# Optimization experiments

Measured on AMD Instinct MI355X. Metric: run time of the kernel, lower is better.

## Reference

```python
import jax, jax.numpy as jnp
import numpy as np

B, H, W, C = 4, 64, 64, 256
CK = C // 8          # 32, f/g projection dim
COUT = 256           # channels_out


def setup_inputs() -> dict:
    key = jax.random.key(0)
    ks = jax.random.split(key, 6)
    s = lambda fan_in: 1.0 / np.sqrt(fan_in)
    return {
        "x": jax.random.normal(ks[0], (B, H, W, C), dtype=jnp.float32),
        "Wf": jax.random.normal(ks[1], (C, CK), dtype=jnp.float32) * s(C),
        "bf": jnp.zeros((CK,), dtype=jnp.float32),
        "Wg": jax.random.normal(ks[2], (C, CK), dtype=jnp.float32) * s(C),
        "bg": jnp.zeros((CK,), dtype=jnp.float32),
        "Wh": jax.random.normal(ks[3], (C, COUT), dtype=jnp.float32) * s(C),
        "bh": jnp.zeros((COUT,), dtype=jnp.float32),
        "Wo": jax.random.normal(ks[4], (COUT, COUT), dtype=jnp.float32) * s(COUT),
        "bo": jnp.zeros((COUT,), dtype=jnp.float32),
        "gamma": jnp.zeros((1,), dtype=jnp.float32),
    }


def reference(x, Wf, bf, Wg, bg, Wh, bh, Wo, bo, gamma):
    b, h, w, c = x.shape
    n = h * w
    xf = x.reshape(b, n, c)                       # [B, N, C]
    # 1x1 convs == per-location dense projections
    f = xf @ Wf + bf                              # [B, N, CK]
    g = xf @ Wg + bg                              # [B, N, CK]
    hh = xf @ Wh + bh                             # [B, N, COUT]
    scores = jnp.einsum("bqk,bnk->bqn", f, g)    # [B, N, N]
    probs = jax.nn.softmax(scores, axis=-1)
    attn = jnp.einsum("bqn,bnd->bqd", probs, hh)  # [B, N, COUT]
    o = attn @ Wo + bo                            # [B, N, COUT]
    y = gamma * o.reshape(b, h, w, -1) + x
    return y
```

## Files before the change

kernel.cpp:

```cpp
#include <hip/hip_runtime.h>
#include <stdint.h>

typedef __attribute__((ext_vector_type(4))) float f32x4;
typedef __attribute__((ext_vector_type(2))) float f32x2;
typedef __attribute__((ext_vector_type(8))) short bf16x8;
typedef __attribute__((ext_vector_type(4))) unsigned short u16x4;

#define NB 4
#define NN 4096
#define CC 256

__device__ __forceinline__ unsigned short f2bf(float f) {
  union { float f; unsigned int u; } v; v.f = f;
  unsigned int u = v.u;
  return (unsigned short)((u + 0x7FFFu + ((u >> 16) & 1u)) >> 16);
}
__device__ __forceinline__ float bf2f(unsigned short h) {
  union { unsigned int u; float f; } v; v.u = ((unsigned int)h) << 16;
  return v.f;
}

typedef __attribute__((address_space(1))) void as1_void;
typedef __attribute__((address_space(3))) void as3_void;
__device__ __forceinline__ void gload_lds16(const unsigned short* g, unsigned short* l) {
  __builtin_amdgcn_global_load_lds((as1_void*)(void*)g, (as3_void*)(void*)l, 16, 0, 0);
}

__global__ __launch_bounds__(64) void k_wprep(
    const float* __restrict__ Wf, const float* __restrict__ Wg,
    const float* __restrict__ Wh, const float* __restrict__ Wo,
    unsigned short* __restrict__ wT, unsigned short* __restrict__ woT)
{
  const int n = blockIdx.x;
  const int l = threadIdx.x;
  const float* src; int nout, col; unsigned short* dst; int drow;
  if (n < 32)       { src = Wf; nout = 32;  col = n;       dst = wT;  drow = n; }
  else if (n < 64)  { src = Wg; nout = 32;  col = n - 32;  dst = wT;  drow = n; }
  else if (n < 320) { src = Wh; nout = 256; col = n - 64;  dst = wT;  drow = n; }
  else              { src = Wo; nout = 256; col = n - 320; dst = woT; drow = n - 320; }
  u16x4 v;
  #pragma unroll
  for (int j = 0; j < 4; ++j)
    v[j] = f2bf(src[(size_t)(4 * l + j) * nout + col]);
  *(u16x4*)&dst[(size_t)drow * 256 + 4 * l] = v;
}

__global__ __launch_bounds__(256) void k_proj(
    const float* __restrict__ x, const unsigned short* __restrict__ wT,
    const float* __restrict__ bf_, const float* __restrict__ bg_,
    const float* __restrict__ bh_,
    unsigned short* __restrict__ fo, unsigned short* __restrict__ go,
    unsigned short* __restrict__ vT)
{
  __shared__ __align__(16) unsigned short xs[32][264];

  const int t = threadIdx.x, w = t >> 6, l = t & 63;
  const int h = l >> 4, q = l & 15;
  const int bid = blockIdx.x;
  const int rt = (bid & 7) * 64 + (bid >> 3);
  const int r0 = rt * 32;

  #pragma unroll
  for (int p = 0; p < 8; ++p) {
    int idx = t + (p << 8);
    int rr = idx >> 6, c4 = (idx & 63) << 2;
    f32x4 v = *(const f32x4*)&x[(size_t)(r0 + rr) * 256 + c4];
    u16x4 o;
    #pragma unroll
    for (int j = 0; j < 4; ++j) o[j] = f2bf(v[j]);
    *(u16x4*)&xs[rr][c4] = o;
  }
  __syncthreads();

  const f32x4 zero = {0.f, 0.f, 0.f, 0.f};
  f32x4 acc[2][5];
  #pragma unroll
  for (int mf = 0; mf < 2; ++mf)
    #pragma unroll
    for (int nf = 0; nf < 5; ++nf) acc[mf][nf] = zero;

  #pragma unroll
  for (int ks = 0; ks < 8; ++ks) {
    bf16x8 a0 = *(const bf16x8*)&xs[q][ks * 32 + 8 * h];
    bf16x8 a1 = *(const bf16x8*)&xs[16 + q][ks * 32 + 8 * h];
    #pragma unroll
    for (int nf = 0; nf < 5; ++nf) {
      bf16x8 b = *(const bf16x8*)&wT[(size_t)(80 * w + 16 * nf + q) * 256 + ks * 32 + 8 * h];
      acc[0][nf] = __builtin_amdgcn_mfma_f32_16x16x32_bf16(a0, b, acc[0][nf], 0, 0, 0);
      acc[1][nf] = __builtin_amdgcn_mfma_f32_16x16x32_bf16(a1, b, acc[1][nf], 0, 0, 0);
    }
  }

  __syncthreads();

  #pragma unroll
  for (int nf = 0; nf < 5; ++nf) {
    const int colb = 80 * w + 16 * nf;
    const int colq = colb + q;
    #pragma unroll
    for (int mf = 0; mf < 2; ++mf) {
      #pragma unroll
      for (int i = 0; i < 4; ++i) {
        int lr = 16 * mf + 4 * h + i;
        float val = acc[mf][nf][i];
        if (colb < 32) {
          fo[(size_t)(r0 + lr) * 32 + colq] =
              f2bf((val + bf_[colq]) * 1.44269504088896f);
        } else if (colb < 64) {
          go[(size_t)(r0 + lr) * 32 + (colq - 32)] = f2bf(val + bg_[colq - 32]);
        } else {
          xs[lr][colq - 64] = f2bf(val + bh_[colq - 64]);
        }
      }
    }
  }
  __syncthreads();

  const int tile = rt >> 1, sfix = rt & 1;
  unsigned short* dst = vT + (size_t)tile * 16384;
  #pragma unroll
  for (int p = 0; p < 4; ++p) {
    int ci = t + (p << 8);
    int dt = ci >> 6, ll = ci & 63;
    int h2 = (ci >> 4) & 3, q2 = ci & 15;
    bf16x8 v;
    #pragma unroll
    for (int i = 0; i < 8; ++i)
      v[i] = (short)xs[8 * h2 + i][dt * 16 + q2];
    *(bf16x8*)&dst[(size_t)(dt * 128 + sfix * 64 + ll) * 8] = v;
  }
}

#define SM_FIXED_MAX 72.0f

__global__ __launch_bounds__(256, 2) void k_attn(
    const unsigned short* __restrict__ fq,
    const unsigned short* __restrict__ gk,
    const unsigned short* __restrict__ vT,
    float* __restrict__ attn)
{
  __shared__ __align__(16) unsigned short vbuf[2][16384];
  __shared__ __align__(16) unsigned short pbuf[2][2048];
  __shared__ float lred[4][2][16];

  const int bid = blockIdx.x;
  const int b  = (bid & 7) >> 1;
  const int qt = (bid >> 3) + ((bid & 1) << 6);
  const int t = threadIdx.x, w = t >> 6, l = t & 63;
  const int h = l >> 4, q = l & 15;
  const int qrow = qt * 32;

  bf16x8 afrag[2];
  #pragma unroll
  for (int u = 0; u < 2; ++u)
    afrag[u] = *(const bf16x8*)&fq[((size_t)b * NN + qrow + u * 16 + q) * 32 + 8 * h];

  const f32x4 zero = {0.f, 0.f, 0.f, 0.f};
  f32x4 acc[2][4];
  #pragma unroll
  for (int u = 0; u < 2; ++u)
    #pragma unroll
    for (int dl = 0; dl < 4; ++dl) acc[u][dl] = zero;
  float lrow[2][4];
  #pragma unroll
  for (int u = 0; u < 2; ++u)
    #pragma unroll
    for (int i = 0; i < 4; ++i) lrow[u][i] = 0.f;

  const unsigned short* gbase = gk + (size_t)b * NN * 32;
  const unsigned short* vbase = vT + (size_t)b * 64 * 16384;

  const int kcol = w * 16 + q;
  const int ps = kcol >> 5, ph2 = (kcol & 31) >> 3, pi2 = kcol & 7;

  {
    const unsigned short* src = vbase + (size_t)w * 4096 + l * 8;
    unsigned short* dst = &vbuf[0][w * 4096];
    #pragma unroll
    for (int i2 = 0; i2 < 8; ++i2)
      gload_lds16(src + i2 * 512, dst + i2 * 512);
  }
  bf16x8 bfj = *(const bf16x8*)&gbase[(size_t)(w * 16 + q) * 32 + 8 * h];
  __syncthreads();

  #pragma unroll 1
  for (int kt = 0; kt < 64; ++kt) {
    const int cur = kt & 1;

    f32x4 s0 = __builtin_amdgcn_mfma_f32_16x16x32_bf16(afrag[0], bfj, zero, 0, 0, 0);
    f32x4 s1 = __builtin_amdgcn_mfma_f32_16x16x32_bf16(afrag[1], bfj, zero, 0, 0, 0);

    bf16x8 bfn = bfj;
    if (kt < 63)
      bfn = *(const bf16x8*)&gbase[(size_t)((kt + 1) * 64 + w * 16 + q) * 32 + 8 * h];

    #pragma unroll
    for (int i = 0; i < 4; ++i) {
      float p0 = exp2f(s0[i] - SM_FIXED_MAX);
      float p1 = exp2f(s1[i] - SM_FIXED_MAX);
      lrow[0][i] += p0;
      lrow[1][i] += p1;
      int slot = (ph2 * 16 + 4 * h + i) * 8 + pi2;
      pbuf[cur][(0 + ps) * 512 + slot] = (unsigned short)(__float_as_uint(p0) >> 16);
      pbuf[cur][(2 + ps) * 512 + slot] = (unsigned short)(__float_as_uint(p1) >> 16);
    }

    __syncthreads();

    if (kt < 63) {
      const unsigned short* src = vbase + (size_t)(kt + 1) * 16384 + w * 4096 + l * 8;
      unsigned short* dst = &vbuf[cur ^ 1][w * 4096];
      #pragma unroll
      for (int i2 = 0; i2 < 8; ++i2)
        gload_lds16(src + i2 * 512, dst + i2 * 512);
    }

    bf16x8 pa[2][2];
    #pragma unroll
    for (int u = 0; u < 2; ++u)
      #pragma unroll
      for (int s2 = 0; s2 < 2; ++s2)
        pa[u][s2] = *(const bf16x8*)&pbuf[cur][(u * 2 + s2) * 512 + l * 8];

    __builtin_amdgcn_s_setprio(1);
    #pragma unroll
    for (int dl = 0; dl < 4; ++dl) {
      const int dt = 4 * w + dl;
      bf16x8 v0 = *(const bf16x8*)&vbuf[cur][dt * 1024 + l * 8];
      bf16x8 v1 = *(const bf16x8*)&vbuf[cur][dt * 1024 + 512 + l * 8];
      acc[0][dl] = __builtin_amdgcn_mfma_f32_16x16x32_bf16(pa[0][0], v0, acc[0][dl], 0, 0, 0);
      acc[1][dl] = __builtin_amdgcn_mfma_f32_16x16x32_bf16(pa[1][0], v0, acc[1][dl], 0, 0, 0);
      acc[0][dl] = __builtin_amdgcn_mfma_f32_16x16x32_bf16(pa[0][1], v1, acc[0][dl], 0, 0, 0);
      acc[1][dl] = __builtin_amdgcn_mfma_f32_16x16x32_bf16(pa[1][1], v1, acc[1][dl], 0, 0, 0);
    }
    __builtin_amdgcn_s_setprio(0);

    bfj = bfn;
  }

  #pragma unroll
  for (int u = 0; u < 2; ++u)
    #pragma unroll
    for (int i = 0; i < 4; ++i)
      #pragma unroll
      for (int d = 1; d < 16; d <<= 1)
        lrow[u][i] += __shfl_xor(lrow[u][i], d);

  if (q == 0) {
    #pragma unroll
    for (int u = 0; u < 2; ++u)
      #pragma unroll
      for (int i = 0; i < 4; ++i)
        lred[w][u][4 * h + i] = lrow[u][i];
  }
  __syncthreads();

  float rl[2][4];
  #pragma unroll
  for (int u = 0; u < 2; ++u)
    #pragma unroll
    for (int i = 0; i < 4; ++i) {
      int row = 4 * h + i;
      rl[u][i] = 1.0f / (lred[0][u][row] + lred[1][u][row] +
                         lred[2][u][row] + lred[3][u][row]);
    }

  #pragma unroll
  for (int u = 0; u < 2; ++u)
    #pragma unroll
    for (int dl = 0; dl < 4; ++dl) {
      int dt = 4 * w + dl;
      #pragma unroll
      for (int i = 0; i < 4; ++i)
        attn[((size_t)b * NN + qrow + u * 16 + 4 * h + i) * 256 + dt * 16 + q] =
            acc[u][dl][i] * rl[u][i];
    }
}

__global__ __launch_bounds__(256) void k_out(
    const unsigned short* __restrict__ woT, const float* __restrict__ bo,
    const float* __restrict__ gamma, const float* __restrict__ x,
    float* __restrict__ y)
{
  __shared__ __align__(16) unsigned short as_[32][264];

  const int t = threadIdx.x, w = t >> 6, l = t & 63;
  const int h = l >> 4, q = l & 15;
  const int bid = blockIdx.x;
  const int rt = (bid & 7) * 64 + (bid >> 3);
  const int r0 = rt * 32;

  #pragma unroll
  for (int p = 0; p < 8; ++p) {
    int idx = t + (p << 8);
    int rr = idx >> 6, c4 = (idx & 63) << 2;
    f32x4 v = *(const f32x4*)&y[(size_t)(r0 + rr) * 256 + c4];
    u16x4 o;
    #pragma unroll
    for (int j = 0; j < 4; ++j) o[j] = f2bf(v[j]);
    *(u16x4*)&as_[rr][c4] = o;
  }
  __syncthreads();

  const f32x4 zero = {0.f, 0.f, 0.f, 0.f};
  f32x4 acc[2][4];
  #pragma unroll
  for (int mf = 0; mf < 2; ++mf)
    #pragma unroll
    for (int nf = 0; nf < 4; ++nf) acc[mf][nf] = zero;

  #pragma unroll
  for (int ks = 0; ks < 8; ++ks) {
    bf16x8 a0 = *(const bf16x8*)&as_[q][ks * 32 + 8 * h];
    bf16x8 a1 = *(const bf16x8*)&as_[16 + q][ks * 32 + 8 * h];
    #pragma unroll
    for (int nf = 0; nf < 4; ++nf) {
      bf16x8 b = *(const bf16x8*)&woT[(size_t)(64 * w + 16 * nf + q) * 256 + ks * 32 + 8 * h];
      acc[0][nf] = __builtin_amdgcn_mfma_f32_16x16x32_bf16(a0, b, acc[0][nf], 0, 0, 0);
      acc[1][nf] = __builtin_amdgcn_mfma_f32_16x16x32_bf16(a1, b, acc[1][nf], 0, 0, 0);
    }
  }

  const float gm = gamma[0];
  #pragma unroll
  for (int mf = 0; mf < 2; ++mf)
    #pragma unroll
    for (int nf = 0; nf < 4; ++nf) {
      int col = 64 * w + 16 * nf + q;
      #pragma unroll
      for (int i = 0; i < 4; ++i) {
        size_t off = (size_t)(r0 + 16 * mf + 4 * h + i) * 256 + col;
        y[off] = gm * (acc[mf][nf][i] + bo[col]) + x[off];
      }
    }
}

extern "C" void kernel_launch(void* const* d_in, const int* in_sizes, int n_in,
                              void* d_out, int out_size, void* d_ws, size_t ws_size,
                              hipStream_t stream) {
  const float* x     = (const float*)d_in[0];
  const float* Wf    = (const float*)d_in[1];
  const float* bf_   = (const float*)d_in[2];
  const float* Wg    = (const float*)d_in[3];
  const float* bg_   = (const float*)d_in[4];
  const float* Wh    = (const float*)d_in[5];
  const float* bh_   = (const float*)d_in[6];
  const float* Wo    = (const float*)d_in[7];
  const float* bo    = (const float*)d_in[8];
  const float* gamma = (const float*)d_in[9];

  unsigned short* f   = (unsigned short*)d_ws;
  unsigned short* g   = f   + (size_t)16384 * 32;
  unsigned short* vT  = g   + (size_t)16384 * 32;
  unsigned short* wT  = vT  + (size_t)16384 * 256;
  unsigned short* woT = wT  + (size_t)320 * 256;

  float* attn = (float*)d_out;

  k_wprep<<<576, 64, 0, stream>>>(Wf, Wg, Wh, Wo, wT, woT);
  k_proj<<<512, 256, 0, stream>>>(x, wT, bf_, bg_, bh_, f, g, vT);
  k_attn<<<512, 256, 0, stream>>>(f, g, vT, attn);
  k_out<<<512, 256, 0, stream>>>(woT, bo, gamma, x, attn);
}
```

Baseline: 113.6 us.

## Load V tiles directly into registers instead of staging through LDS

The attention kernel now loads each warp's slice of the V tile straight from global memory into register double-buffers (vA/vB) rather than staging it in a 64KB LDS buffer via global_load_lds. The loop is unrolled by two with a macro so the register buffers swap statically. This removes the LDS V traffic and the shared-memory footprint, which may allow higher occupancy. In exchange it raises register pressure (16 extra bf16x8 vectors) under launch_bounds(256,2), and global-load latency is now exposed directly in registers.

Result: faster. 110.6 us (-2.7%).

```diff
diff --git a/kernel.cpp b/kernel.cpp
--- a/kernel.cpp
+++ b/kernel.cpp
@@ -18,12 +18,6 @@
 __device__ __forceinline__ float bf2f(unsigned short h) {
   union { unsigned int u; float f; } v; v.u = ((unsigned int)h) << 16;
   return v.f;
-}
-
-typedef __attribute__((address_space(1))) void as1_void;
-typedef __attribute__((address_space(3))) void as3_void;
-__device__ __forceinline__ void gload_lds16(const unsigned short* g, unsigned short* l) {
-  __builtin_amdgcn_global_load_lds((as1_void*)(void*)g, (as3_void*)(void*)l, 16, 0, 0);
 }
 
 __global__ __launch_bounds__(64) void k_wprep(
@@ -133,13 +127,55 @@
 
 #define SM_FIXED_MAX 72.0f
 
+#define ATTN_TILE(KT, VCUR, VNXT, CUR)                                          \
+  {                                                                             \
+                                        \
+    f32x4 s0 = __builtin_amdgcn_mfma_f32_16x16x32_bf16(afrag[0], bfj, zero, 0, 0, 0); \
+    f32x4 s1 = __builtin_amdgcn_mfma_f32_16x16x32_bf16(afrag[1], bfj, zero, 0, 0, 0); \
+    if ((KT) < 63)                                                              \
+      bfj = *(const bf16x8*)&gbase[(size_t)(((KT) + 1) * 64 + w * 16 + q) * 32 + 8 * h]; \
+          \
+    _Pragma("unroll")                                                           \
+    for (int i = 0; i < 4; ++i) {                                               \
+      float p0 = exp2f(s0[i] - SM_FIXED_MAX);                                   \
+      float p1 = exp2f(s1[i] - SM_FIXED_MAX);                                   \
+      lrow[0][i] += p0;                                                         \
+      lrow[1][i] += p1;                                                         \
+      int slot = (ph2 * 16 + 4 * h + i) * 8 + pi2;                              \
+      pbuf[CUR][ps * 512 + slot]       = (unsigned short)(__float_as_uint(p0) >> 16); \
+      pbuf[CUR][(2 + ps) * 512 + slot] = (unsigned short)(__float_as_uint(p1) >> 16); \
+    }                                                                           \
+    __syncthreads();                \
+       \
+    if ((KT) < 63) {                                                            \
+      const unsigned short* vs =                                                \
+          vbase + (size_t)((KT) + 1) * 16384 + w * 4096 + l * 8;                \
+      _Pragma("unroll")                                                         \
+      for (int i2 = 0; i2 < 8; ++i2)                                            \
+        VNXT[i2] = *(const bf16x8*)(vs + i2 * 512);                             \
+    }                                                                           \
+                                                        \
+    bf16x8 pa00 = *(const bf16x8*)&pbuf[CUR][0 * 512 + l * 8];                  \
+    bf16x8 pa01 = *(const bf16x8*)&pbuf[CUR][1 * 512 + l * 8];                  \
+    bf16x8 pa10 = *(const bf16x8*)&pbuf[CUR][2 * 512 + l * 8];                  \
+    bf16x8 pa11 = *(const bf16x8*)&pbuf[CUR][3 * 512 + l * 8];                  \
+    __builtin_amdgcn_s_setprio(1);                                              \
+    _Pragma("unroll")                                                           \
+    for (int dl = 0; dl < 4; ++dl) {                                            \
+      acc[0][dl] = __builtin_amdgcn_mfma_f32_16x16x32_bf16(pa00, VCUR[2 * dl],     acc[0][dl], 0, 0, 0); \
+      acc[1][dl] = __builtin_amdgcn_mfma_f32_16x16x32_bf16(pa10, VCUR[2 * dl],     acc[1][dl], 0, 0, 0); \
+      acc[0][dl] = __builtin_amdgcn_mfma_f32_16x16x32_bf16(pa01, VCUR[2 * dl + 1], acc[0][dl], 0, 0, 0); \
+      acc[1][dl] = __builtin_amdgcn_mfma_f32_16x16x32_bf16(pa11, VCUR[2 * dl + 1], acc[1][dl], 0, 0, 0); \
+    }                                                                           \
+    __builtin_amdgcn_s_setprio(0);                                              \
+  }
+
 __global__ __launch_bounds__(256, 2) void k_attn(
     const unsigned short* __restrict__ fq,
     const unsigned short* __restrict__ gk,
     const unsigned short* __restrict__ vT,
     float* __restrict__ attn)
 {
-  __shared__ __align__(16) unsigned short vbuf[2][16384];
   __shared__ __align__(16) unsigned short pbuf[2][2048];
   __shared__ float lred[4][2][16];
 
@@ -173,69 +209,19 @@
   const int kcol = w * 16 + q;
   const int ps = kcol >> 5, ph2 = (kcol & 31) >> 3, pi2 = kcol & 7;
 
+  bf16x8 vA[8], vB[8];
   {
-    const unsigned short* src = vbase + (size_t)w * 4096 + l * 8;
-    unsigned short* dst = &vbuf[0][w * 4096];
+    const unsigned short* vs = vbase + (size_t)w * 4096 + l * 8;
     #pragma unroll
     for (int i2 = 0; i2 < 8; ++i2)
-      gload_lds16(src + i2 * 512, dst + i2 * 512);
+      vA[i2] = *(const bf16x8*)(vs + i2 * 512);
   }
   bf16x8 bfj = *(const bf16x8*)&gbase[(size_t)(w * 16 + q) * 32 + 8 * h];
-  __syncthreads();
 
   #pragma unroll 1
-  for (int kt = 0; kt < 64; ++kt) {
-    const int cur = kt & 1;
-
-    f32x4 s0 = __builtin_amdgcn_mfma_f32_16x16x32_bf16(afrag[0], bfj, zero, 0, 0, 0);
-    f32x4 s1 = __builtin_amdgcn_mfma_f32_16x16x32_bf16(afrag[1], bfj, zero, 0, 0, 0);
-
-    bf16x8 bfn = bfj;
-    if (kt < 63)
-      bfn = *(const bf16x8*)&gbase[(size_t)((kt + 1) * 64 + w * 16 + q) * 32 + 8 * h];
-
-    #pragma unroll
-    for (int i = 0; i < 4; ++i) {
-      float p0 = exp2f(s0[i] - SM_FIXED_MAX);
-      float p1 = exp2f(s1[i] - SM_FIXED_MAX);
-      lrow[0][i] += p0;
-      lrow[1][i] += p1;
-      int slot = (ph2 * 16 + 4 * h + i) * 8 + pi2;
-      pbuf[cur][(0 + ps) * 512 + slot] = (unsigned short)(__float_as_uint(p0) >> 16);
-      pbuf[cur][(2 + ps) * 512 + slot] = (unsigned short)(__float_as_uint(p1) >> 16);
-    }
-
-    __syncthreads();
-
-    if (kt < 63) {
-      const unsigned short* src = vbase + (size_t)(kt + 1) * 16384 + w * 4096 + l * 8;
-      unsigned short* dst = &vbuf[cur ^ 1][w * 4096];
-      #pragma unroll
-      for (int i2 = 0; i2 < 8; ++i2)
-        gload_lds16(src + i2 * 512, dst + i2 * 512);
-    }
-
-    bf16x8 pa[2][2];
-    #pragma unroll
-    for (int u = 0; u < 2; ++u)
-      #pragma unroll
-      for (int s2 = 0; s2 < 2; ++s2)
-        pa[u][s2] = *(const bf16x8*)&pbuf[cur][(u * 2 + s2) * 512 + l * 8];
-
-    __builtin_amdgcn_s_setprio(1);
-    #pragma unroll
-    for (int dl = 0; dl < 4; ++dl) {
-      const int dt = 4 * w + dl;
-      bf16x8 v0 = *(const bf16x8*)&vbuf[cur][dt * 1024 + l * 8];
-      bf16x8 v1 = *(const bf16x8*)&vbuf[cur][dt * 1024 + 512 + l * 8];
-      acc[0][dl] = __builtin_amdgcn_mfma_f32_16x16x32_bf16(pa[0][0], v0, acc[0][dl], 0, 0, 0);
-      acc[1][dl] = __builtin_amdgcn_mfma_f32_16x16x32_bf16(pa[1][0], v0, acc[1][dl], 0, 0, 0);
-      acc[0][dl] = __builtin_amdgcn_mfma_f32_16x16x32_bf16(pa[0][1], v1, acc[0][dl], 0, 0, 0);
-      acc[1][dl] = __builtin_amdgcn_mfma_f32_16x16x32_bf16(pa[1][1], v1, acc[1][dl], 0, 0, 0);
-    }
-    __builtin_amdgcn_s_setprio(0);
-
-    bfj = bfn;
+  for (int kt = 0; kt < 64; kt += 2) {
+    ATTN_TILE(kt,     vA, vB, 0);
+    ATTN_TILE(kt + 1, vB, vA, 1);
   }
 
   #pragma unroll
```
